# Kernel tuning notes

Measured on AMD Instinct MI355X. Metric: run time of the kernel, lower is better.

The kernel has to match this reference:

```python
import jax, jax.numpy as jnp
import numpy as np

N_NODES = 10000


def _add_self_loops(edge_index, n):
    loops = jnp.arange(n, dtype=edge_index.dtype)
    row = jnp.concatenate([edge_index[0], loops])
    col = jnp.concatenate([edge_index[1], loops])
    return row, col


def _gcn_norm(row, col, n):
    # symmetric normalization: deg^-1/2[row] * deg^-1/2[col], deg counted on col
    deg = jax.ops.segment_sum(jnp.ones_like(col, dtype=jnp.float32), col, num_segments=n)
    dis = jnp.where(deg > 0, jax.lax.rsqrt(jnp.maximum(deg, 1.0)), 0.0)
    return dis[row] * dis[col]


def _gcn_conv(x, W, b, row, col, norm, n):
    h = x @ W                      # [N, out]
    m = h[row] * norm[:, None]     # [E+N, out] gathered, normalized messages
    out = jax.ops.segment_sum(m, col, num_segments=n)
    return out + b


def setup_inputs() -> dict:
    key = jax.random.key(0)
    ks = jax.random.split(key, 10)
    N, E, Cin, Cout = N_NODES, 160000, 256, 512
    x = jax.random.normal(ks[0], (N, Cin), dtype=jnp.float32)
    edge_index = jax.random.randint(ks[1], (2, E), 0, N, dtype=jnp.int64)
    s = 1.0 / np.sqrt(Cin)
    s2 = 1.0 / np.sqrt(Cout)
    return {
        "x": x,
        "edge_index": edge_index,
        "W1": jax.random.normal(ks[2], (Cin, Cout), dtype=jnp.float32) * s,
        "b1": jnp.zeros((Cout,), dtype=jnp.float32),
        "W2": jax.random.normal(ks[3], (Cout, Cout), dtype=jnp.float32) * s2,
        "b2": jnp.zeros((Cout,), dtype=jnp.float32),
        "W3": jax.random.normal(ks[4], (Cout, Cout), dtype=jnp.float32) * s2,
        "b3": jnp.zeros((Cout,), dtype=jnp.float32),
        "W4": jax.random.normal(ks[5], (Cout, Cout), dtype=jnp.float32) * s2,
        "b4": jnp.zeros((Cout,), dtype=jnp.float32),
    }


def reference(x, edge_index, W1, b1, W2, b2, W3, b3, W4, b4):
    n = x.shape[0]
    row, col = _add_self_loops(edge_index, n)
    norm = _gcn_norm(row, col, n)
    h = jax.nn.relu(_gcn_conv(x, W1, b1, row, col, norm, n))
    h = jax.nn.relu(_gcn_conv(h, W2, b2, row, col, norm, n))
    h = jax.nn.relu(_gcn_conv(h, W3, b3, row, col, norm, n))
    h = _gcn_conv(h, W4, b4, row, col, norm, n)
    return h.reshape(-1, 5, h.shape[-1])  # [N/5, 5, 512]
```

## Files before the change

### kernel.cpp

```cpp
#include <hip/hip_runtime.h>
#include <hip/hip_bf16.h>

#define N_NODES 10000
#define N_EDGES 160000

typedef __hip_bfloat16 bf16;
typedef unsigned short u16;
typedef float f32x4 __attribute__((ext_vector_type(4)));
typedef short s16x8 __attribute__((ext_vector_type(8)));
typedef unsigned short us8 __attribute__((ext_vector_type(8)));
typedef unsigned short us4 __attribute__((ext_vector_type(4)));

static __device__ __forceinline__ float b2f(u16 u) {
    unsigned v = (unsigned)u << 16;
    return __uint_as_float(v);
}
static __device__ __forceinline__ u16 f2b(float f) {
    bf16 b = __float2bfloat16(f);
    return *reinterpret_cast<u16*>(&b);
}

#define GLDS(gp, lp)                                                         \
    __builtin_amdgcn_global_load_lds(                                        \
        (const __attribute__((address_space(1))) void*)(const void*)(gp),    \
        (__attribute__((address_space(3))) void*)(lp), 16, 0, 0)


__global__ void k_prep0(const int* __restrict__ ei,
                        int* __restrict__ row, int* __restrict__ col,
                        int* __restrict__ deg) {
    bool is64 = true;
#pragma unroll
    for (int i = 0; i < 8; ++i) is64 = is64 && (ei[2 * i + 1] == 0);
    int t = blockIdx.x * 256 + threadIdx.x;
    if (t < N_NODES) deg[t] = 0;
    if (t < N_EDGES) {
        if (is64) {
            row[t] = ei[2 * t];
            col[t] = ei[2 * (N_EDGES + t)];
        } else {
            row[t] = ei[t];
            col[t] = ei[N_EDGES + t];
        }
    }
}

__global__ void k_count(const int* __restrict__ col, int* deg) {
    int e = blockIdx.x * 256 + threadIdx.x;
    if (e < N_EDGES) atomicAdd(&deg[col[e]], 1);
}

__global__ void k_scan_all(const int* __restrict__ deg, float* __restrict__ dis,
                           int* __restrict__ off, int* __restrict__ cur) {
    __shared__ int sums[256];
    int t = threadIdx.x;
    const int seg = (N_NODES + 255) >> 8;
    int lo = t * seg, hi = lo + seg;
    if (lo > N_NODES) lo = N_NODES;
    if (hi > N_NODES) hi = N_NODES;
    int s = 0;
    for (int i = lo; i < hi; ++i) {
        dis[i] = rsqrtf((float)deg[i] + 1.0f);
        s += deg[i];
    }
    sums[t] = s;
    __syncthreads();
    for (int d = 1; d < 256; d <<= 1) {
        int v = (t >= d) ? sums[t - d] : 0;
        __syncthreads();
        sums[t] += v;
        __syncthreads();
    }
    int run = sums[t] - s;
    for (int i = lo; i < hi; ++i) {
        off[i] = run;
        cur[i] = run;
        run += deg[i];
    }
    if (t == 255) off[N_NODES] = sums[255];
}

__global__ void k_fill(const int* __restrict__ row, const int* __restrict__ col,
                       const float* __restrict__ dis, int* cur,
                       int* __restrict__ crow, float* __restrict__ cnorm) {
    int e = blockIdx.x * 256 + threadIdx.x;
    if (e < N_EDGES) {
        int r = row[e], c = col[e];
        int p = atomicAdd(&cur[c], 1);
        crow[p] = r;
        cnorm[p] = dis[r] * dis[c];
    }
}


__global__ void k_convx(const float* __restrict__ x, u16* __restrict__ xb) {
    int i = blockIdx.x * 256 + threadIdx.x;
    float4 v = *(const float4*)(x + (size_t)i * 4);
    us4 st;
    st[0] = f2b(v.x); st[1] = f2b(v.y); st[2] = f2b(v.z); st[3] = f2b(v.w);
    *(us4*)(xb + (size_t)i * 4) = st;
}


__global__ void k_transpose(const float* __restrict__ W1, const float* __restrict__ W2,
                            const float* __restrict__ W3, const float* __restrict__ W4,
                            u16* __restrict__ T1, u16* __restrict__ T2,
                            u16* __restrict__ T3, u16* __restrict__ T4) {
    __shared__ u16 tile[32][33];
    int z = blockIdx.z;
    const float* W = (z == 0) ? W1 : (z == 1) ? W2 : (z == 2) ? W3 : W4;
    u16* WT        = (z == 0) ? T1 : (z == 1) ? T2 : (z == 2) ? T3 : T4;
    int K = (z == 0) ? 256 : 512;
    int k0 = blockIdx.y * 32;
    if (k0 >= K) return;
    int n0 = blockIdx.x * 32;
    int tx = threadIdx.x, ty = threadIdx.y;
    for (int i = 0; i < 32; i += 8)
        tile[ty + i][tx] = f2b(W[(size_t)(k0 + ty + i) * 512 + n0 + tx]);
    __syncthreads();
    for (int i = 0; i < 32; i += 8)
        WT[(size_t)(n0 + ty + i) * K + k0 + tx] = tile[tx][ty + i];
}


template <int CE> struct VecT;
template <> struct VecT<4> { typedef us4 T; };
template <> struct VecT<8> { typedef us8 T; };

template <int CE>
__global__ void k_agg(const u16* __restrict__ in, u16* __restrict__ out,
                      const int* __restrict__ off, const int* __restrict__ crow,
                      const float* __restrict__ cnorm, const float* __restrict__ dis) {
    typedef typename VecT<CE>::T VT;
    const int C = CE * 64;
    int node = blockIdx.x * 4 + (threadIdx.x >> 6);
    int lane = threadIdx.x & 63;
    if (node >= N_NODES) return;
    int c = lane * CE;

    float d = dis[node];
    VT sv = *(const VT*)(in + (size_t)node * C + c);
    float acc[CE], acc2[CE];
#pragma unroll
    for (int j = 0; j < CE; ++j) { acc[j] = b2f(sv[j]) * d * d; acc2[j] = 0.f; }

    int b = off[node], e = off[node + 1];
    int i = b;
    for (; i + 1 < e; i += 2) {
        int r0 = crow[i], r1 = crow[i + 1];
        float n0 = cnorm[i], n1 = cnorm[i + 1];
        VT v0 = *(const VT*)(in + (size_t)r0 * C + c);
        VT v1 = *(const VT*)(in + (size_t)r1 * C + c);
#pragma unroll
        for (int j = 0; j < CE; ++j) {
            acc[j]  = fmaf(b2f(v0[j]), n0, acc[j]);
            acc2[j] = fmaf(b2f(v1[j]), n1, acc2[j]);
        }
    }
    if (i < e) {
        int r0 = crow[i];
        float n0 = cnorm[i];
        VT v0 = *(const VT*)(in + (size_t)r0 * C + c);
#pragma unroll
        for (int j = 0; j < CE; ++j) acc[j] = fmaf(b2f(v0[j]), n0, acc[j]);
    }
    VT st;
#pragma unroll
    for (int j = 0; j < CE; ++j) st[j] = f2b(acc[j] + acc2[j]);
    *(VT*)(out + (size_t)node * C + c) = st;
}


static __device__ __forceinline__ void st_out(float* out, size_t idx, float v) { out[idx] = v; }
static __device__ __forceinline__ void st_out(u16* out, size_t idx, float v) { out[idx] = f2b(v); }

template <typename OT>
__global__ __launch_bounds__(256) void k_gemm(
        const u16* __restrict__ A, const u16* __restrict__ BT,
        const float* __restrict__ bias, OT* __restrict__ out,
        int M, int K, int NO, int relu) {
    __shared__ u16 As[2][64][32];
    __shared__ u16 Bs[2][64][32];

    int tid = threadIdx.x;
    int w = tid >> 6;
    int lane = tid & 63;
    int wm = w >> 1, wn = w & 1;
    int m0 = blockIdx.x * 64;
    int n0 = blockIdx.y * 64;
    int l15 = lane & 15;
    int kq = lane >> 4;

    int sp  = w & 1;
    int srb = (w >> 1) * 32;
    int srow = lane >> 2;
    int skc  = (lane & 3) * 8;

    int ar0 = m0 + srb + srow;      if (ar0 > M - 1) ar0 = M - 1;
    int ar1 = m0 + srb + 16 + srow; if (ar1 > M - 1) ar1 = M - 1;
    int br0 = n0 + srb + srow;
    int br1 = br0 + 16;
    const u16* agp0 = A + (size_t)ar0 * K + sp * 32 + skc;
    const u16* agp1 = A + (size_t)ar1 * K + sp * 32 + skc;
    const u16* bgp0 = BT + (size_t)br0 * K + sp * 32 + skc;
    const u16* bgp1 = BT + (size_t)br1 * K + sp * 32 + skc;
    u16* al0 = &As[sp][srb][0];
    u16* al1 = &As[sp][srb + 16][0];
    u16* bl0 = &Bs[sp][srb][0];
    u16* bl1 = &Bs[sp][srb + 16][0];

    int aRow0 = wm * 32 + l15, aRow1 = aRow0 + 16;
    int bRow0 = wn * 32 + l15, bRow1 = bRow0 + 16;

    f32x4 acc00 = {0.f, 0.f, 0.f, 0.f};
    f32x4 acc01 = acc00, acc10 = acc00, acc11 = acc00;

    for (int k0 = 0; k0 < K; k0 += 64) {
        GLDS(agp0 + k0, al0);
        GLDS(agp1 + k0, al1);
        GLDS(bgp0 + k0, bl0);
        GLDS(bgp1 + k0, bl1);
        __syncthreads();
#pragma unroll
        for (int p = 0; p < 2; ++p) {
            s16x8 a0 = *(const s16x8*)&As[p][aRow0][kq * 8];
            s16x8 a1 = *(const s16x8*)&As[p][aRow1][kq * 8];
            s16x8 b0 = *(const s16x8*)&Bs[p][bRow0][kq * 8];
            s16x8 b1 = *(const s16x8*)&Bs[p][bRow1][kq * 8];
            acc00 = __builtin_amdgcn_mfma_f32_16x16x32_bf16(a0, b0, acc00, 0, 0, 0);
            acc01 = __builtin_amdgcn_mfma_f32_16x16x32_bf16(a0, b1, acc01, 0, 0, 0);
            acc10 = __builtin_amdgcn_mfma_f32_16x16x32_bf16(a1, b0, acc10, 0, 0, 0);
            acc11 = __builtin_amdgcn_mfma_f32_16x16x32_bf16(a1, b1, acc11, 0, 0, 0);
        }
        __syncthreads();
    }

    int r0 = (lane >> 4) * 4;
    int cm0 = m0 + wm * 32;
    int cn0 = n0 + wn * 32;
    float bv0 = bias[cn0 + l15];
    float bv1 = bias[cn0 + 16 + l15];
#pragma unroll
    for (int r = 0; r < 4; ++r) {
        int rowa = cm0 + r0 + r;
        if (rowa < M) {
            float v = acc00[r] + bv0;
            if (relu) v = fmaxf(v, 0.f);
            st_out(out, (size_t)rowa * NO + cn0 + l15, v);
            v = acc01[r] + bv1;
            if (relu) v = fmaxf(v, 0.f);
            st_out(out, (size_t)rowa * NO + cn0 + 16 + l15, v);
        }
        int rowb = rowa + 16;
        if (rowb < M) {
            float v = acc10[r] + bv0;
            if (relu) v = fmaxf(v, 0.f);
            st_out(out, (size_t)rowb * NO + cn0 + l15, v);
            v = acc11[r] + bv1;
            if (relu) v = fmaxf(v, 0.f);
            st_out(out, (size_t)rowb * NO + cn0 + 16 + l15, v);
        }
    }
}


extern "C" void kernel_launch(void* const* d_in, const int* in_sizes, int n_in,
                              void* d_out, int out_size, void* d_ws, size_t ws_size,
                              hipStream_t stream) {
    const float* x  = (const float*)d_in[0];
    const int*   ei = (const int*)d_in[1];
    const float* W1 = (const float*)d_in[2];
    const float* b1 = (const float*)d_in[3];
    const float* W2 = (const float*)d_in[4];
    const float* b2 = (const float*)d_in[5];
    const float* W3 = (const float*)d_in[6];
    const float* b3 = (const float*)d_in[7];
    const float* W4 = (const float*)d_in[8];
    const float* b4 = (const float*)d_in[9];

    char* ws = (char*)d_ws;
    size_t o = 0;
    auto alloc = [&](size_t bytes) {
        char* p = ws + o;
        o = (o + bytes + 255) & ~(size_t)255;
        return p;
    };
    int*   row   = (int*)alloc(N_EDGES * 4);
    int*   col   = (int*)alloc(N_EDGES * 4);
    int*   deg   = (int*)alloc(N_NODES * 4);
    float* dis   = (float*)alloc(N_NODES * 4);
    int*   off   = (int*)alloc((N_NODES + 1) * 4);
    int*   cur   = (int*)alloc(N_NODES * 4);
    int*   crow  = (int*)alloc(N_EDGES * 4);
    float* cnorm = (float*)alloc(N_EDGES * 4);
    u16*   WT1   = (u16*)alloc((size_t)512 * 256 * 2);
    u16*   WT2   = (u16*)alloc((size_t)512 * 512 * 2);
    u16*   WT3   = (u16*)alloc((size_t)512 * 512 * 2);
    u16*   WT4   = (u16*)alloc((size_t)512 * 512 * 2);
    u16*   xb    = (u16*)alloc((size_t)N_NODES * 256 * 2);
    u16*   s     = (u16*)alloc((size_t)N_NODES * 512 * 2);
    u16*   h     = (u16*)alloc((size_t)N_NODES * 512 * 2);
    float* outb  = (float*)d_out;

    dim3 b256(256);
    const int gE = (N_EDGES + 255) / 256;
    const dim3 gG(157, 8);
    const int gA = (N_NODES + 3) / 4;

    k_prep0<<<gE, b256, 0, stream>>>(ei, row, col, deg);
    k_count<<<gE, b256, 0, stream>>>(col, deg);
    k_scan_all<<<1, b256, 0, stream>>>(deg, dis, off, cur);
    k_fill<<<gE, b256, 0, stream>>>(row, col, dis, cur, crow, cnorm);
    k_convx<<<N_NODES * 256 / 4 / 256, b256, 0, stream>>>(x, xb);
    k_transpose<<<dim3(16, 16, 4), dim3(32, 8), 0, stream>>>(W1, W2, W3, W4,
                                                             WT1, WT2, WT3, WT4);

    k_agg<4><<<gA, b256, 0, stream>>>(xb, s, off, crow, cnorm, dis);
    k_gemm<u16><<<gG, b256, 0, stream>>>(s, WT1, b1, h, N_NODES, 256, 512, 1);
    k_agg<8><<<gA, b256, 0, stream>>>(h, s, off, crow, cnorm, dis);
    k_gemm<u16><<<gG, b256, 0, stream>>>(s, WT2, b2, h, N_NODES, 512, 512, 1);
    k_agg<8><<<gA, b256, 0, stream>>>(h, s, off, crow, cnorm, dis);
    k_gemm<u16><<<gG, b256, 0, stream>>>(s, WT3, b3, h, N_NODES, 512, 512, 1);
    k_agg<8><<<gA, b256, 0, stream>>>(h, s, off, crow, cnorm, dis);
    k_gemm<float><<<gG, b256, 0, stream>>>(s, WT4, b4, outb, N_NODES, 512, 512, 0);
}
```

Baseline: 296.3 us.

## Split aggregation across channel chunks, unroll edges by four, widen GEMM K-step

The aggregation kernel now splits each 512-wide node row across two wavefronts that each handle a 256-channel chunk. It also unrolls the edge loop four-wide with four independent accumulators, so more gathers are in flight at once. The GEMM stages 128 K-elements per barrier instead of 64, using four LDS slices with each wave loading one slice, which halves the number of syncs. The cost is doubled LDS use per block and redundant per-node offset and dis reads across the chunk wavefronts.

```diff
diff --git a/kernel.cpp b/kernel.cpp
--- a/kernel.cpp
+++ b/kernel.cpp
@@ -24,6 +24,10 @@
     __builtin_amdgcn_global_load_lds(                                        \
         (const __attribute__((address_space(1))) void*)(const void*)(gp),    \
         (__attribute__((address_space(3))) void*)(lp), 16, 0, 0)
+
+template <int CE> struct VecSel;
+template <> struct VecSel<4> { typedef us4 T; };
+template <> struct VecSel<8> { typedef us8 T; };
 
 
 __global__ void k_prep0(const int* __restrict__ ei,
@@ -92,7 +96,6 @@
     }
 }
 
-
 __global__ void k_convx(const float* __restrict__ x, u16* __restrict__ xb) {
     int i = blockIdx.x * 256 + threadIdx.x;
     float4 v = *(const float4*)(x + (size_t)i * 4);
@@ -100,7 +103,6 @@
     st[0] = f2b(v.x); st[1] = f2b(v.y); st[2] = f2b(v.z); st[3] = f2b(v.w);
     *(us4*)(xb + (size_t)i * 4) = st;
 }
-
 
 __global__ void k_transpose(const float* __restrict__ W1, const float* __restrict__ W2,
                             const float* __restrict__ W3, const float* __restrict__ W4,
@@ -123,50 +125,55 @@
 }
 
 
-template <int CE> struct VecT;
-template <> struct VecT<4> { typedef us4 T; };
-template <> struct VecT<8> { typedef us8 T; };
-
-template <int CE>
+template <int C, int NCH>
 __global__ void k_agg(const u16* __restrict__ in, u16* __restrict__ out,
                       const int* __restrict__ off, const int* __restrict__ crow,
                       const float* __restrict__ cnorm, const float* __restrict__ dis) {
-    typedef typename VecT<CE>::T VT;
-    const int C = CE * 64;
-    int node = blockIdx.x * 4 + (threadIdx.x >> 6);
+    const int CE = C / (64 * NCH);
+    typedef typename VecSel<CE>::T VT;
+    int wid = blockIdx.x * 4 + (threadIdx.x >> 6);
     int lane = threadIdx.x & 63;
+    int node = wid / NCH;
     if (node >= N_NODES) return;
-    int c = lane * CE;
+    int ch = wid % NCH;
+    int c = ch * (CE * 64) + lane * CE;
 
     float d = dis[node];
     VT sv = *(const VT*)(in + (size_t)node * C + c);
-    float acc[CE], acc2[CE];
-#pragma unroll
-    for (int j = 0; j < CE; ++j) { acc[j] = b2f(sv[j]) * d * d; acc2[j] = 0.f; }
+    float a0[CE], a1[CE], a2[CE], a3[CE];
+#pragma unroll
+    for (int j = 0; j < CE; ++j) {
+        a0[j] = b2f(sv[j]) * d * d;
+        a1[j] = 0.f; a2[j] = 0.f; a3[j] = 0.f;
+    }
 
     int b = off[node], e = off[node + 1];
     int i = b;
-    for (; i + 1 < e; i += 2) {
-        int r0 = crow[i], r1 = crow[i + 1];
-        float n0 = cnorm[i], n1 = cnorm[i + 1];
+    for (; i + 3 < e; i += 4) {
+        int r0 = crow[i], r1 = crow[i + 1], r2 = crow[i + 2], r3 = crow[i + 3];
+        float n0 = cnorm[i], n1 = cnorm[i + 1], n2 = cnorm[i + 2], n3 = cnorm[i + 3];
         VT v0 = *(const VT*)(in + (size_t)r0 * C + c);
         VT v1 = *(const VT*)(in + (size_t)r1 * C + c);
+        VT v2 = *(const VT*)(in + (size_t)r2 * C + c);
+        VT v3 = *(const VT*)(in + (size_t)r3 * C + c);
 #pragma unroll
         for (int j = 0; j < CE; ++j) {
-            acc[j]  = fmaf(b2f(v0[j]), n0, acc[j]);
-            acc2[j] = fmaf(b2f(v1[j]), n1, acc2[j]);
-        }
-    }
-    if (i < e) {
+            a0[j] = fmaf(b2f(v0[j]), n0, a0[j]);
+            a1[j] = fmaf(b2f(v1[j]), n1, a1[j]);
+            a2[j] = fmaf(b2f(v2[j]), n2, a2[j]);
+            a3[j] = fmaf(b2f(v3[j]), n3, a3[j]);
+        }
+    }
+    for (; i < e; ++i) {
         int r0 = crow[i];
         float n0 = cnorm[i];
         VT v0 = *(const VT*)(in + (size_t)r0 * C + c);
 #pragma unroll
-        for (int j = 0; j < CE; ++j) acc[j] = fmaf(b2f(v0[j]), n0, acc[j]);
+        for (int j = 0; j < CE; ++j) a0[j] = fmaf(b2f(v0[j]), n0, a0[j]);
     }
     VT st;
 #pragma unroll
-    for (int j = 0; j < CE; ++j) st[j] = f2b(acc[j] + acc2[j]);
+    for (int j = 0; j < CE; ++j) st[j] = f2b((a0[j] + a1[j]) + (a2[j] + a3[j]));
     *(VT*)(out + (size_t)node * C + c) = st;
 }
 
@@ -179,8 +186,8 @@
         const u16* __restrict__ A, const u16* __restrict__ BT,
         const float* __restrict__ bias, OT* __restrict__ out,
         int M, int K, int NO, int relu) {
-    __shared__ u16 As[2][64][32];
-    __shared__ u16 Bs[2][64][32];
+    __shared__ u16 As[4][64][32];
+    __shared__ u16 Bs[4][64][32];
 
     int tid = threadIdx.x;
     int w = tid >> 6;
@@ -191,23 +198,20 @@
     int l15 = lane & 15;
     int kq = lane >> 4;
 
-    int sp  = w & 1;
-    int srb = (w >> 1) * 32;
     int srow = lane >> 2;
     int skc  = (lane & 3) * 8;
-
-    int ar0 = m0 + srb + srow;      if (ar0 > M - 1) ar0 = M - 1;
-    int ar1 = m0 + srb + 16 + srow; if (ar1 > M - 1) ar1 = M - 1;
-    int br0 = n0 + srb + srow;
-    int br1 = br0 + 16;
-    const u16* agp0 = A + (size_t)ar0 * K + sp * 32 + skc;
-    const u16* agp1 = A + (size_t)ar1 * K + sp * 32 + skc;
-    const u16* bgp0 = BT + (size_t)br0 * K + sp * 32 + skc;
-    const u16* bgp1 = BT + (size_t)br1 * K + sp * 32 + skc;
-    u16* al0 = &As[sp][srb][0];
-    u16* al1 = &As[sp][srb + 16][0];
-    u16* bl0 = &Bs[sp][srb][0];
-    u16* bl1 = &Bs[sp][srb + 16][0];
+    const u16* agp[4];
+    const u16* bgp[4];
+    u16* al[4];
+    u16* bl[4];
+#pragma unroll
+    for (int j = 0; j < 4; ++j) {
+        int arw = m0 + j * 16 + srow; if (arw > M - 1) arw = M - 1;
+        agp[j] = A + (size_t)arw * K + w * 32 + skc;
+        bgp[j] = BT + (size_t)(n0 + j * 16 + srow) * K + w * 32 + skc;
+        al[j] = &As[w][j * 16][0];
+        bl[j] = &Bs[w][j * 16][0];
+    }
 
     int aRow0 = wm * 32 + l15, aRow1 = aRow0 + 16;
     int bRow0 = wn * 32 + l15, bRow1 = bRow0 + 16;
@@ -215,14 +219,14 @@
     f32x4 acc00 = {0.f, 0.f, 0.f, 0.f};
     f32x4 acc01 = acc00, acc10 = acc00, acc11 = acc00;
 
-    for (int k0 = 0; k0 < K; k0 += 64) {
-        GLDS(agp0 + k0, al0);
-        GLDS(agp1 + k0, al1);
-        GLDS(bgp0 + k0, bl0);
-        GLDS(bgp1 + k0, bl1);
+    for (int k0 = 0; k0 < K; k0 += 128) {
+#pragma unroll
+        for (int j = 0; j < 4; ++j) GLDS(agp[j] + k0, al[j]);
+#pragma unroll
+        for (int j = 0; j < 4; ++j) GLDS(bgp[j] + k0, bl[j]);
         __syncthreads();
 #pragma unroll
-        for (int p = 0; p < 2; ++p) {
+        for (int p = 0; p < 4; ++p) {
             s16x8 a0 = *(const s16x8*)&As[p][aRow0][kq * 8];
             s16x8 a1 = *(const s16x8*)&As[p][aRow1][kq * 8];
             s16x8 b0 = *(const s16x8*)&Bs[p][bRow0][kq * 8];
@@ -305,7 +309,8 @@
     dim3 b256(256);
     const int gE = (N_EDGES + 255) / 256;
     const dim3 gG(157, 8);
-    const int gA = (N_NODES + 3) / 4;
+    const int gA1 = (N_NODES + 3) / 4;
+    const int gA2 = (N_NODES * 2 + 3) / 4;
 
     k_prep0<<<gE, b256, 0, stream>>>(ei, row, col, deg);
     k_count<<<gE, b256, 0, stream>>>(col, deg);
@@ -315,12 +320,12 @@
     k_transpose<<<dim3(16, 16, 4), dim3(32, 8), 0, stream>>>(W1, W2, W3, W4,
                                                              WT1, WT2, WT3, WT4);
 
-    k_agg<4><<<gA, b256, 0, stream>>>(xb, s, off, crow, cnorm, dis);
+    k_agg<256, 1><<<gA1, b256, 0, stream>>>(xb, s, off, crow, cnorm, dis);
     k_gemm<u16><<<gG, b256, 0, stream>>>(s, WT1, b1, h, N_NODES, 256, 512, 1);
-    k_agg<8><<<gA, b256, 0, stream>>>(h, s, off, crow, cnorm, dis);
+    k_agg<512, 2><<<gA2, b256, 0, stream>>>(h, s, off, crow, cnorm, dis);
     k_gemm<u16><<<gG, b256, 0, stream>>>(s, WT2, b2, h, N_NODES, 512, 512, 1);
-    k_agg<8><<<gA, b256, 0, stream>>>(h, s, off, crow, cnorm, dis);
+    k_agg<512, 2><<<gA2, b256, 0, stream>>>(h, s, off, crow, cnorm, dis);
     k_gemm<u16><<<gG, b256, 0, stream>>>(s, WT3, b3, h, N_NODES, 512, 512, 1);
-    k_agg<8><<<gA, b256, 0, stream>>>(h, s, off, crow, cnorm, dis);
+    k_agg<512, 2><<<gA2, b256, 0, stream>>>(h, s, off, crow, cnorm, dis);
     k_gemm<float><<<gG, b256, 0, stream>>>(s, WT4, b4, outb, N_NODES, 512, 512, 0);
 }
```

Measured after the change: 300.7 us. No clear change (+1.5%).
